# Optimization experiments

Hardware: AMD Instinct MI355X
Metric: run time of the kernel (lower is better)

## Reference

```python
import jax, jax.numpy as jnp
import numpy as np

HEAD_DIM = 128
NUM_BUCKETS = 32
MAX_DISTANCE = 128


def _rel_pos_bucket(seq_len):
    # T5 causal relative-position bucketing (lucidrains flash-pytorch version)
    pos = jnp.arange(seq_len)
    rel = pos[None, :] - pos[:, None]          # k_pos - q_pos
    n = jnp.maximum(-rel, 0)                   # causal: only past distances
    max_exact = NUM_BUCKETS // 2
    is_small = n < max_exact
    n_safe = jnp.maximum(n, 1).astype(jnp.float32)
    val_large = max_exact + (
        jnp.log(n_safe / max_exact) / np.log(MAX_DISTANCE / max_exact)
        * (NUM_BUCKETS - max_exact)
    ).astype(jnp.int32)
    val_large = jnp.minimum(val_large, NUM_BUCKETS - 1)
    return jnp.where(is_small, n, val_large)   # (S, S) int32


def setup_inputs() -> dict:
    key = jax.random.key(0)
    ks = jax.random.split(key, 10)
    B, S, D, I = 4, 2048, 768, 1536
    s = 0.02
    return {
        "x": jax.random.normal(ks[0], (B, S, D), jnp.float32),
        "v_W": jax.random.normal(ks[1], (D, I), jnp.float32) * s,
        "v_b": jnp.zeros((I,), jnp.float32),
        "g_W": jax.random.normal(ks[2], (D, I), jnp.float32) * s,
        "g_b": jnp.zeros((I,), jnp.float32),
        "in_W": jax.random.normal(ks[3], (D, HEAD_DIM), jnp.float32) * s,
        "in_b": jnp.zeros((HEAD_DIM,), jnp.float32),
        "q_gamma": jax.random.normal(ks[4], (HEAD_DIM,), jnp.float32) * s,
        "q_beta": jnp.zeros((HEAD_DIM,), jnp.float32),
        "k_gamma": jax.random.normal(ks[5], (HEAD_DIM,), jnp.float32) * s,
        "k_beta": jnp.zeros((HEAD_DIM,), jnp.float32),
        "out_W": jax.random.normal(ks[6], (I, D), jnp.float32) * s,
        "out_b": jnp.zeros((D,), jnp.float32),
        "rel_emb": jax.random.normal(ks[7], (NUM_BUCKETS, 1), jnp.float32) * s,
    }


def reference(x, v_W, v_b, g_W, g_b, in_W, in_b,
              q_gamma, q_beta, k_gamma, k_beta, out_W, out_b, rel_emb):
    silu = jax.nn.silu
    S = x.shape[1]
    v = silu(x @ v_W + v_b)                    # (B, S, I)
    gate = silu(x @ g_W + g_b)                 # (B, S, I)
    base = silu(x @ in_W + in_b)               # (B, S, 128)
    q = base * q_gamma + q_beta
    k = base * k_gamma + k_beta
    # scores scaled by sqrt(v dim) per torch code (v.size(-1) = inner_dim)
    attn = jnp.einsum('bns,bms->bnm', q, k) / jnp.sqrt(jnp.float32(v.shape[-1]))
    bias = rel_emb[_rel_pos_bucket(S), 0] * np.sqrt(HEAD_DIM)  # (S, S)
    attn = attn + bias
    causal = jnp.triu(jnp.ones((S, S), bool), 1)
    attn = jnp.where(causal, 0.0, attn)        # masked_fill to 0 before relu^2
    attn = jnp.square(jax.nn.relu(attn))       # ReLU^2 attention (no softmax)
    o = jnp.einsum('bnm,bme->bne', attn, v) * gate
    return o @ out_W + out_b                   # (B, S, D)
```

## Files before the change

kernel.cpp:

```cpp
#include <hip/hip_runtime.h>


typedef short short8 __attribute__((ext_vector_type(8)));
typedef float f32x4 __attribute__((ext_vector_type(4)));
typedef unsigned short us4 __attribute__((ext_vector_type(4)));
typedef float fl4 __attribute__((ext_vector_type(4)));

__device__ __forceinline__ unsigned short f2bf(float f) {
  unsigned u = __builtin_bit_cast(unsigned, f);
  u += 0x7FFFu + ((u >> 16) & 1u);
  return (unsigned short)(u >> 16);
}
__device__ __forceinline__ float bf2f(unsigned short b) {
  return __builtin_bit_cast(float, ((unsigned)b) << 16);
}
__device__ __forceinline__ float silu_f(float x) { return x / (1.0f + __expf(-x)); }

__device__ __forceinline__ void gl_lds16(const void* gp, void* lp) {
  __builtin_amdgcn_global_load_lds((const __attribute__((address_space(1))) void*)gp,
                                   (__attribute__((address_space(3))) void*)lp, 16, 0, 0);
}

__device__ __forceinline__ void stage_bf(const unsigned short* __restrict__ g,
                                         int row_stride, int r0, int ko,
                                         unsigned short* lds, int w, int l) {
#pragma unroll
  for (int c = 0; c < 4; ++c) {
    int e = ((w * 4 + c) << 9) + l * 8;
    gl_lds16(g + (size_t)(r0 + (e >> 6)) * row_stride + (ko + (e & 63)), lds + e);
  }
}
__device__ __forceinline__ void stage_bf64(const unsigned short* __restrict__ g,
                                           int row_stride, int r0, int ko,
                                           unsigned short* lds, int w, int l) {
#pragma unroll
  for (int c = 0; c < 2; ++c) {
    int e = ((w * 2 + c) << 9) + l * 8;
    gl_lds16(g + (size_t)(r0 + (e >> 6)) * row_stride + (ko + (e & 63)), lds + e);
  }
}

__device__ __forceinline__ void mfma_bf(const unsigned short* As, const unsigned short* Bs,
                                        f32x4 acc[4][4], int wm, int wn, int quad, int lc) {
#pragma unroll
  for (int kk = 0; kk < 2; ++kk) {
    short8 af[4], bfr[4];
#pragma unroll
    for (int i = 0; i < 4; ++i)
      af[i] = *(const short8*)&As[(wm + i * 16 + lc) * 64 + kk * 32 + quad * 8];
#pragma unroll
    for (int j = 0; j < 4; ++j)
      bfr[j] = *(const short8*)&Bs[(wn + j * 16 + lc) * 64 + kk * 32 + quad * 8];
#pragma unroll
    for (int i = 0; i < 4; ++i)
#pragma unroll
      for (int j = 0; j < 4; ++j)
        acc[i][j] = __builtin_amdgcn_mfma_f32_16x16x32_bf16(af[i], bfr[j], acc[i][j], 0, 0, 0);
  }
}

__global__ __launch_bounds__(256) void g123_k(
    const unsigned short* __restrict__ X,
    const unsigned short* __restrict__ Wst,
    unsigned short* __restrict__ vt,
    unsigned short* __restrict__ gateT,
    unsigned short* __restrict__ wq,
    unsigned short* __restrict__ wk,
    const float* __restrict__ v_b, const float* __restrict__ g_b,
    const float* __restrict__ in_b, const float* __restrict__ q_g,
    const float* __restrict__ q_be, const float* __restrict__ k_g,
    const float* __restrict__ k_be) {
  __shared__ unsigned short As[2][128 * 64];
  __shared__ unsigned short Bs[2][128 * 64];
  const int t = threadIdx.x, l = t & 63, w = t >> 6;
  const int id = blockIdx.x;
  const int xcd = id & 7, rest = id >> 3;
  const int n = rest % 25, m = (rest / 25) * 8 + xcd;
  const int m0 = m * 128, n0 = n * 128;
  const int wm = (w >> 1) * 64, wn = (w & 1) * 64;
  const int quad = l >> 4, lr = quad * 4, lc = l & 15;

  f32x4 acc[4][4] = {};
  stage_bf(X, 768, m0, 0, As[0], w, l);
  stage_bf(Wst, 768, n0, 0, Bs[0], w, l);
  __syncthreads();
  int cur = 0;
  for (int tt = 1; tt < 12; ++tt) {
    stage_bf(X, 768, m0, tt * 64, As[cur ^ 1], w, l);
    stage_bf(Wst, 768, n0, tt * 64, Bs[cur ^ 1], w, l);
    mfma_bf(As[cur], Bs[cur], acc, wm, wn, quad, lc);
    __syncthreads();
    cur ^= 1;
  }
  mfma_bf(As[cur], Bs[cur], acc, wm, wn, quad, lc);

#pragma unroll
  for (int i = 0; i < 4; ++i) {
    const int gm = m0 + wm + i * 16 + lr;
#pragma unroll
    for (int j = 0; j < 4; ++j) {
      const int gn = n0 + wn + j * 16 + lc;
      f32x4 a = acc[i][j];
      if (n0 < 1536) {
        float bv = v_b[gn];
        us4 pk;
#pragma unroll
        for (int r = 0; r < 4; ++r) pk[r] = f2bf(silu_f(a[r] + bv));
        size_t off = (size_t)(gm >> 11) * (1536 * 2048) + (size_t)gn * 2048 + (gm & 2047);
        *(us4*)&vt[off] = pk;
      } else if (n0 < 3072) {
        float bv = g_b[gn - 1536];
        us4 pk;
#pragma unroll
        for (int r = 0; r < 4; ++r) pk[r] = f2bf(silu_f(a[r] + bv));
        *(us4*)&gateT[(size_t)(gn - 1536) * 8192 + gm] = pk;
      } else {
        int h = gn - 3072;
        float bb = in_b[h], qg = q_g[h], qb = q_be[h], kg = k_g[h], kb = k_be[h];
#pragma unroll
        for (int r = 0; r < 4; ++r) {
          float s = silu_f(a[r] + bb);
          wq[(size_t)(gm + r) * 128 + h] = f2bf(s * qg + qb);
          wk[(size_t)(gm + r) * 128 + h] = f2bf(s * kg + kb);
        }
      }
    }
  }
}

__global__ __launch_bounds__(256) void scores_k(
    const unsigned short* __restrict__ wk, const unsigned short* __restrict__ wq,
    unsigned short* __restrict__ P, const float* __restrict__ btab) {
  __shared__ unsigned short As[128 * 128];
  __shared__ unsigned short Bs[128 * 128];
  const int t = threadIdx.x, l = t & 63, w = t >> 6;
  const int z = blockIdx.z;
  int ti = blockIdx.x;
  int r = (int)((sqrtf((float)(8 * ti + 1)) - 1.0f) * 0.5f);
  if ((r + 1) * (r + 2) / 2 <= ti) ++r;
  int c = ti - r * (r + 1) / 2;
  const int m0 = c * 128, n0 = r * 128;
  const unsigned short* A = wk + (size_t)z * 2048 * 128;
  const unsigned short* Bt = wq + (size_t)z * 2048 * 128;
  unsigned short* Pz = P + (size_t)z * 2048 * 2048;
  const int wm = (w >> 1) * 64, wn = (w & 1) * 64;
  const int quad = l >> 4, lr = quad * 4, lc = l & 15;

#pragma unroll
  for (int cc = 0; cc < 8; ++cc) {
    int e = ((w * 8 + cc) << 9) + l * 8;
    gl_lds16(A + (size_t)(m0 + (e >> 7)) * 128 + (e & 127), As + e);
  }
#pragma unroll
  for (int cc = 0; cc < 8; ++cc) {
    int e = ((w * 8 + cc) << 9) + l * 8;
    gl_lds16(Bt + (size_t)(n0 + (e >> 7)) * 128 + (e & 127), Bs + e);
  }
  __syncthreads();

  f32x4 acc[4][4] = {};
#pragma unroll
  for (int kk = 0; kk < 4; ++kk) {
    short8 af[4], bfr[4];
#pragma unroll
    for (int i = 0; i < 4; ++i)
      af[i] = *(const short8*)&As[(wm + i * 16 + lc) * 128 + kk * 32 + quad * 8];
#pragma unroll
    for (int j = 0; j < 4; ++j)
      bfr[j] = *(const short8*)&Bs[(wn + j * 16 + lc) * 128 + kk * 32 + quad * 8];
#pragma unroll
    for (int i = 0; i < 4; ++i)
#pragma unroll
      for (int j = 0; j < 4; ++j)
        acc[i][j] = __builtin_amdgcn_mfma_f32_16x16x32_bf16(af[i], bfr[j], acc[i][j], 0, 0, 0);
  }

  const float SCALE = 0.025515518153991442f;
#pragma unroll
  for (int i = 0; i < 4; ++i) {
    const int gm = m0 + wm + i * 16 + lr;
#pragma unroll
    for (int j = 0; j < 4; ++j) {
      const int gn = n0 + wn + j * 16 + lc;
      us4 pk;
#pragma unroll
      for (int r2 = 0; r2 < 4; ++r2) {
        int mm = gm + r2;
        float v = 0.0f;
        if (mm <= gn) {
          float tt = fmaf(acc[i][j][r2], SCALE, btab[gn - mm]);
          tt = fmaxf(tt, 0.0f);
          v = tt * tt;
        }
        pk[r2] = f2bf(v);
      }
      *(us4*)&Pz[(size_t)gn * 2048 + gm] = pk;
    }
  }
}

__global__ __launch_bounds__(256) void og_k(
    const unsigned short* __restrict__ Vt,
    const unsigned short* __restrict__ P,
    const unsigned short* __restrict__ gateT,
    unsigned short* __restrict__ og) {
  __shared__ unsigned short As[2][128 * 64];
  __shared__ unsigned short Bs[2][128 * 64];
  const int t = threadIdx.x, l = t & 63, w = t >> 6;
  const int id = blockIdx.x;
  const int bblk = id / 96, rr = id % 96;
  const int xcd = rr & 7, mi = rr >> 3;
  const int half = xcd >> 2, z = xcd & 3;
  const int nt = 15 - 2 * bblk - (half ^ (bblk & 1));
  const int m0 = mi * 128;
  const int n0 = nt * 128;
  const int T = (n0 + 128) >> 6;
  const unsigned short* A = Vt + (size_t)z * 1536 * 2048;
  const unsigned short* B = P + (size_t)z * 2048 * 2048;
  const int wm = (w >> 1) * 64, wn = (w & 1) * 64;
  const int quad = l >> 4, lr = quad * 4, lc = l & 15;

  f32x4 acc[4][4] = {};
  stage_bf(A, 2048, m0, 0, As[0], w, l);
  stage_bf(B, 2048, n0, 0, Bs[0], w, l);
  __syncthreads();
  int cur = 0;
  for (int tt = 1; tt < T; ++tt) {
    stage_bf(A, 2048, m0, tt * 64, As[cur ^ 1], w, l);
    stage_bf(B, 2048, n0, tt * 64, Bs[cur ^ 1], w, l);
    mfma_bf(As[cur], Bs[cur], acc, wm, wn, quad, lc);
    __syncthreads();
    cur ^= 1;
  }
  mfma_bf(As[cur], Bs[cur], acc, wm, wn, quad, lc);

#pragma unroll
  for (int i = 0; i < 4; ++i) {
    const int gm = m0 + wm + i * 16 + lr;
#pragma unroll
    for (int j = 0; j < 4; ++j) {
      const int gn = n0 + wn + j * 16 + lc;
      us4 pk;
#pragma unroll
      for (int r2 = 0; r2 < 4; ++r2) {
        float g = bf2f(gateT[(size_t)(gm + r2) * 8192 + z * 2048 + gn]);
        pk[r2] = f2bf(acc[i][j][r2] * g);
      }
      *(us4*)&og[((size_t)z * 2048 + gn) * 1536 + gm] = pk;
    }
  }
}

__global__ __launch_bounds__(256) void gout_k(
    const unsigned short* __restrict__ A,
    const unsigned short* __restrict__ Bt,
    float* __restrict__ out, const float* __restrict__ o_b) {
  __shared__ unsigned short As[2][64 * 64];
  __shared__ unsigned short Bs[2][128 * 64];
  const int t = threadIdx.x, l = t & 63, w = t >> 6;
  const int id = blockIdx.x;
  const int xcd = id & 7, rest = id >> 3;
  const int m = rest % 12, ng = rest / 12;
  const int m0 = m * 64, n0 = (ng * 8 + xcd) * 128;
  const int wm = (w >> 1) * 32, wn = (w & 1) * 64;
  const int quad = l >> 4, lr = quad * 4, lc = l & 15;

  f32x4 acc[2][4] = {};
  stage_bf64(A, 1536, m0, 0, As[0], w, l);
  stage_bf(Bt, 1536, n0, 0, Bs[0], w, l);
  __syncthreads();
  int cur = 0;
  for (int tt = 1; tt < 24; ++tt) {
    stage_bf64(A, 1536, m0, tt * 64, As[cur ^ 1], w, l);
    stage_bf(Bt, 1536, n0, tt * 64, Bs[cur ^ 1], w, l);
#pragma unroll
    for (int kk = 0; kk < 2; ++kk) {
      short8 af[2], bfr[4];
#pragma unroll
      for (int i = 0; i < 2; ++i)
        af[i] = *(const short8*)&As[cur][(wm + i * 16 + lc) * 64 + kk * 32 + quad * 8];
#pragma unroll
      for (int j = 0; j < 4; ++j)
        bfr[j] = *(const short8*)&Bs[cur][(wn + j * 16 + lc) * 64 + kk * 32 + quad * 8];
#pragma unroll
      for (int i = 0; i < 2; ++i)
#pragma unroll
        for (int j = 0; j < 4; ++j)
          acc[i][j] = __builtin_amdgcn_mfma_f32_16x16x32_bf16(af[i], bfr[j], acc[i][j], 0, 0, 0);
    }
    __syncthreads();
    cur ^= 1;
  }
#pragma unroll
  for (int kk = 0; kk < 2; ++kk) {
    short8 af[2], bfr[4];
#pragma unroll
    for (int i = 0; i < 2; ++i)
      af[i] = *(const short8*)&As[cur][(wm + i * 16 + lc) * 64 + kk * 32 + quad * 8];
#pragma unroll
    for (int j = 0; j < 4; ++j)
      bfr[j] = *(const short8*)&Bs[cur][(wn + j * 16 + lc) * 64 + kk * 32 + quad * 8];
#pragma unroll
    for (int i = 0; i < 2; ++i)
#pragma unroll
      for (int j = 0; j < 4; ++j)
        acc[i][j] = __builtin_amdgcn_mfma_f32_16x16x32_bf16(af[i], bfr[j], acc[i][j], 0, 0, 0);
  }

#pragma unroll
  for (int i = 0; i < 2; ++i) {
    const int gm = m0 + wm + i * 16 + lr;
#pragma unroll
    for (int j = 0; j < 4; ++j) {
      const int gn = n0 + wn + j * 16 + lc;
      fl4 ob = *(const fl4*)&o_b[gm];
      fl4 res;
#pragma unroll
      for (int r2 = 0; r2 < 4; ++r2) res[r2] = acc[i][j][r2] + ob[r2];
      *(fl4*)&out[(size_t)gn * 768 + gm] = res;
    }
  }
}

__global__ void cvt_bf16(const float* __restrict__ in, unsigned short* __restrict__ out, int n) {
  int i = (blockIdx.x * blockDim.x + threadIdx.x) * 4;
  if (i < n) {
    fl4 v = *(const fl4*)&in[i];
    us4 o;
#pragma unroll
    for (int r = 0; r < 4; ++r) o[r] = f2bf(v[r]);
    *(us4*)&out[i] = o;
  }
}

__global__ void transpose_cvt4(const float* __restrict__ s0, unsigned short* __restrict__ d0,
                               const float* __restrict__ s1, unsigned short* __restrict__ d1,
                               const float* __restrict__ s2, unsigned short* __restrict__ d2,
                               const float* __restrict__ s3, unsigned short* __restrict__ d3) {
  __shared__ float tile[32][33];
  const float* in;
  unsigned short* out;
  int K_, N_, bxm, bym;
  switch (blockIdx.z) {
    case 0: in = s0; out = d0; K_ = 768; N_ = 1536; bxm = 48; bym = 24; break;
    case 1: in = s1; out = d1; K_ = 768; N_ = 1536; bxm = 48; bym = 24; break;
    case 2: in = s2; out = d2; K_ = 768; N_ = 128;  bxm = 4;  bym = 24; break;
    default: in = s3; out = d3; K_ = 1536; N_ = 768; bxm = 24; bym = 48; break;
  }
  if ((int)blockIdx.x >= bxm || (int)blockIdx.y >= bym) return;
  int bn = blockIdx.x * 32, bk = blockIdx.y * 32;
  int tx = threadIdx.x, ty = threadIdx.y;
#pragma unroll
  for (int i2 = 0; i2 < 32; i2 += 8)
    tile[ty + i2][tx] = in[(size_t)(bk + ty + i2) * N_ + (bn + tx)];
  __syncthreads();
#pragma unroll
  for (int i2 = 0; i2 < 32; i2 += 8)
    out[(size_t)(bn + ty + i2) * K_ + (bk + tx)] = f2bf(tile[tx][ty + i2]);
}

__global__ void build_bias(const float* __restrict__ rel_emb, float* __restrict__ tab) {
  int d = blockIdx.x * blockDim.x + threadIdx.x;
  if (d < 2048) {
    int bucket;
    if (d < 16) {
      bucket = d;
    } else {
      float n = (float)d;
      int vl = 16 + (int)((logf(n * 0.0625f) / logf(8.0f)) * 16.0f);
      bucket = vl < 31 ? vl : 31;
    }
    tab[d] = rel_emb[bucket] * 11.3137085f;
  }
}

extern "C" void kernel_launch(void* const* d_in, const int* in_sizes, int n_in,
                              void* d_out, int out_size, void* d_ws, size_t ws_size,
                              hipStream_t stream) {
  const float* x    = (const float*)d_in[0];
  const float* vW   = (const float*)d_in[1];
  const float* v_b  = (const float*)d_in[2];
  const float* gW   = (const float*)d_in[3];
  const float* g_b  = (const float*)d_in[4];
  const float* inW  = (const float*)d_in[5];
  const float* in_b = (const float*)d_in[6];
  const float* q_g  = (const float*)d_in[7];
  const float* q_be = (const float*)d_in[8];
  const float* k_g  = (const float*)d_in[9];
  const float* k_be = (const float*)d_in[10];
  const float* oW   = (const float*)d_in[11];
  const float* o_b  = (const float*)d_in[12];
  const float* rel  = (const float*)d_in[13];

  char* p = (char*)d_ws;
  auto alloc = [&](size_t bytes) -> char* {
    char* r = p;
    p += (bytes + 255) & ~(size_t)255;
    return r;
  };
  unsigned short* x_bf   = (unsigned short*)alloc(8192ull * 768 * 2);
  unsigned short* wstack = (unsigned short*)alloc(3200ull * 768 * 2);
  unsigned short* vWt  = wstack;
  unsigned short* gWt  = wstack + 1536ull * 768;
  unsigned short* inWt = wstack + 3072ull * 768;
  unsigned short* oWt  = (unsigned short*)alloc(768ull * 1536 * 2);
  unsigned short* wq   = (unsigned short*)alloc(8192ull * 128 * 2);
  unsigned short* wk   = (unsigned short*)alloc(8192ull * 128 * 2);
  unsigned short* vt   = (unsigned short*)alloc(4ull * 1536 * 2048 * 2);
  unsigned short* gateT= (unsigned short*)alloc(1536ull * 8192 * 2);
  unsigned short* P    = (unsigned short*)alloc(4ull * 2048 * 2048 * 2);
  unsigned short* og   = (unsigned short*)alloc(8192ull * 1536 * 2);
  float* btab          = (float*)alloc(2048 * 4);

  cvt_bf16<<<dim3(6144), dim3(256), 0, stream>>>(x, x_bf, 8192 * 768);
  transpose_cvt4<<<dim3(48, 48, 4), dim3(32, 8), 0, stream>>>(vW, vWt, gW, gWt, inW, inWt, oW, oWt);
  build_bias<<<dim3(8), dim3(256), 0, stream>>>(rel, btab);

  g123_k<<<dim3(1600), 256, 0, stream>>>(x_bf, wstack, vt, gateT, wq, wk,
                                         v_b, g_b, in_b, q_g, q_be, k_g, k_be);
  scores_k<<<dim3(136, 1, 4), 256, 0, stream>>>(wk, wq, P, btab);
  og_k<<<dim3(768), 256, 0, stream>>>(vt, P, gateT, og);
  gout_k<<<dim3(768), 256, 0, stream>>>(oWt, og, (float*)d_out, o_b);
}
```

Baseline: 336.8 us.

## Enlarge g123 M-tile, drop LDS double buffering, fuse bias table build

The projection GEMM now computes 256x128 tiles per block with 8x4 accumulators per wave and launches half as many blocks, with a two-blocks-per-CU occupancy hint. The g123, og and gout kernels drop double-buffered LDS staging in favour of a single buffer with load, sync, compute, sync, which halves LDS use so more blocks can be resident. The bias-table kernel is folded into the transpose kernel as an extra z-slice, removing one launch. The cost is that loads no longer overlap MFMA within a block, so latency hiding relies on running more blocks at once. The larger accumulator set also raises register pressure.

```diff
diff --git a/kernel.cpp b/kernel.cpp
--- a/kernel.cpp
+++ b/kernel.cpp
@@ -30,6 +30,15 @@
     gl_lds16(g + (size_t)(r0 + (e >> 6)) * row_stride + (ko + (e & 63)), lds + e);
   }
 }
+__device__ __forceinline__ void stage_bf256(const unsigned short* __restrict__ g,
+                                            int row_stride, int r0, int ko,
+                                            unsigned short* lds, int w, int l) {
+#pragma unroll
+  for (int c = 0; c < 8; ++c) {
+    int e = ((w * 8 + c) << 9) + l * 8;
+    gl_lds16(g + (size_t)(r0 + (e >> 6)) * row_stride + (ko + (e & 63)), lds + e);
+  }
+}
 __device__ __forceinline__ void stage_bf64(const unsigned short* __restrict__ g,
                                            int row_stride, int r0, int ko,
                                            unsigned short* lds, int w, int l) {
@@ -59,7 +68,7 @@
   }
 }
 
-__global__ __launch_bounds__(256) void g123_k(
+__global__ __launch_bounds__(256, 2) void g123_k(
     const unsigned short* __restrict__ X,
     const unsigned short* __restrict__ Wst,
     unsigned short* __restrict__ vt,
@@ -70,32 +79,41 @@
     const float* __restrict__ in_b, const float* __restrict__ q_g,
     const float* __restrict__ q_be, const float* __restrict__ k_g,
     const float* __restrict__ k_be) {
-  __shared__ unsigned short As[2][128 * 64];
-  __shared__ unsigned short Bs[2][128 * 64];
+  __shared__ unsigned short As[256 * 64];
+  __shared__ unsigned short Bs[128 * 64];
   const int t = threadIdx.x, l = t & 63, w = t >> 6;
   const int id = blockIdx.x;
   const int xcd = id & 7, rest = id >> 3;
   const int n = rest % 25, m = (rest / 25) * 8 + xcd;
-  const int m0 = m * 128, n0 = n * 128;
-  const int wm = (w >> 1) * 64, wn = (w & 1) * 64;
+  const int m0 = m * 256, n0 = n * 128;
+  const int wm = (w >> 1) * 128, wn = (w & 1) * 64;
   const int quad = l >> 4, lr = quad * 4, lc = l & 15;
 
-  f32x4 acc[4][4] = {};
-  stage_bf(X, 768, m0, 0, As[0], w, l);
-  stage_bf(Wst, 768, n0, 0, Bs[0], w, l);
-  __syncthreads();
-  int cur = 0;
-  for (int tt = 1; tt < 12; ++tt) {
-    stage_bf(X, 768, m0, tt * 64, As[cur ^ 1], w, l);
-    stage_bf(Wst, 768, n0, tt * 64, Bs[cur ^ 1], w, l);
-    mfma_bf(As[cur], Bs[cur], acc, wm, wn, quad, lc);
-    __syncthreads();
-    cur ^= 1;
-  }
-  mfma_bf(As[cur], Bs[cur], acc, wm, wn, quad, lc);
-
-#pragma unroll
-  for (int i = 0; i < 4; ++i) {
+  f32x4 acc[8][4] = {};
+  for (int ko = 0; ko < 768; ko += 64) {
+    stage_bf256(X, 768, m0, ko, As, w, l);
+    stage_bf(Wst, 768, n0, ko, Bs, w, l);
+    __syncthreads();
+#pragma unroll
+    for (int kk = 0; kk < 2; ++kk) {
+      short8 af[8], bfr[4];
+#pragma unroll
+      for (int i = 0; i < 8; ++i)
+        af[i] = *(const short8*)&As[(wm + i * 16 + lc) * 64 + kk * 32 + quad * 8];
+#pragma unroll
+      for (int j = 0; j < 4; ++j)
+        bfr[j] = *(const short8*)&Bs[(wn + j * 16 + lc) * 64 + kk * 32 + quad * 8];
+#pragma unroll
+      for (int i = 0; i < 8; ++i)
+#pragma unroll
+        for (int j = 0; j < 4; ++j)
+          acc[i][j] = __builtin_amdgcn_mfma_f32_16x16x32_bf16(af[i], bfr[j], acc[i][j], 0, 0, 0);
+    }
+    __syncthreads();
+  }
+
+#pragma unroll
+  for (int i = 0; i < 8; ++i) {
     const int gm = m0 + wm + i * 16 + lr;
 #pragma unroll
     for (int j = 0; j < 4; ++j) {
@@ -204,8 +222,8 @@
     const unsigned short* __restrict__ P,
     const unsigned short* __restrict__ gateT,
     unsigned short* __restrict__ og) {
-  __shared__ unsigned short As[2][128 * 64];
-  __shared__ unsigned short Bs[2][128 * 64];
+  __shared__ unsigned short As[128 * 64];
+  __shared__ unsigned short Bs[128 * 64];
   const int t = threadIdx.x, l = t & 63, w = t >> 6;
   const int id = blockIdx.x;
   const int bblk = id / 96, rr = id % 96;
@@ -214,26 +232,20 @@
   const int nt = 15 - 2 * bblk - (half ^ (bblk & 1));
   const int m0 = mi * 128;
   const int n0 = nt * 128;
-  const int T = (n0 + 128) >> 6;
+  const int kend = n0 + 128;
   const unsigned short* A = Vt + (size_t)z * 1536 * 2048;
   const unsigned short* B = P + (size_t)z * 2048 * 2048;
   const int wm = (w >> 1) * 64, wn = (w & 1) * 64;
   const int quad = l >> 4, lr = quad * 4, lc = l & 15;
 
   f32x4 acc[4][4] = {};
-  stage_bf(A, 2048, m0, 0, As[0], w, l);
-  stage_bf(B, 2048, n0, 0, Bs[0], w, l);
-  __syncthreads();
-  int cur = 0;
-  for (int tt = 1; tt < T; ++tt) {
-    stage_bf(A, 2048, m0, tt * 64, As[cur ^ 1], w, l);
-    stage_bf(B, 2048, n0, tt * 64, Bs[cur ^ 1], w, l);
-    mfma_bf(As[cur], Bs[cur], acc, wm, wn, quad, lc);
-    __syncthreads();
-    cur ^= 1;
-  }
-  mfma_bf(As[cur], Bs[cur], acc, wm, wn, quad, lc);
-
+  for (int ko = 0; ko < kend; ko += 64) {
+    stage_bf(A, 2048, m0, ko, As, w, l);
+    stage_bf(B, 2048, n0, ko, Bs, w, l);
+    __syncthreads();
+    mfma_bf(As, Bs, acc, wm, wn, quad, lc);
+    __syncthreads();
+  }
 #pragma unroll
   for (int i = 0; i < 4; ++i) {
     const int gm = m0 + wm + i * 16 + lr;
@@ -255,8 +267,8 @@
     const unsigned short* __restrict__ A,
     const unsigned short* __restrict__ Bt,
     float* __restrict__ out, const float* __restrict__ o_b) {
-  __shared__ unsigned short As[2][64 * 64];
-  __shared__ unsigned short Bs[2][128 * 64];
+  __shared__ unsigned short As[64 * 64];
+  __shared__ unsigned short Bs[128 * 64];
   const int t = threadIdx.x, l = t & 63, w = t >> 6;
   const int id = blockIdx.x;
   const int xcd = id & 7, rest = id >> 3;
@@ -266,22 +278,19 @@
   const int quad = l >> 4, lr = quad * 4, lc = l & 15;
 
   f32x4 acc[2][4] = {};
-  stage_bf64(A, 1536, m0, 0, As[0], w, l);
-  stage_bf(Bt, 1536, n0, 0, Bs[0], w, l);
-  __syncthreads();
-  int cur = 0;
-  for (int tt = 1; tt < 24; ++tt) {
-    stage_bf64(A, 1536, m0, tt * 64, As[cur ^ 1], w, l);
-    stage_bf(Bt, 1536, n0, tt * 64, Bs[cur ^ 1], w, l);
+  for (int ko = 0; ko < 1536; ko += 64) {
+    stage_bf64(A, 1536, m0, ko, As, w, l);
+    stage_bf(Bt, 1536, n0, ko, Bs, w, l);
+    __syncthreads();
 #pragma unroll
     for (int kk = 0; kk < 2; ++kk) {
       short8 af[2], bfr[4];
 #pragma unroll
       for (int i = 0; i < 2; ++i)
-        af[i] = *(const short8*)&As[cur][(wm + i * 16 + lc) * 64 + kk * 32 + quad * 8];
+        af[i] = *(const short8*)&As[(wm + i * 16 + lc) * 64 + kk * 32 + quad * 8];
 #pragma unroll
       for (int j = 0; j < 4; ++j)
-        bfr[j] = *(const short8*)&Bs[cur][(wn + j * 16 + lc) * 64 + kk * 32 + quad * 8];
+        bfr[j] = *(const short8*)&Bs[(wn + j * 16 + lc) * 64 + kk * 32 + quad * 8];
 #pragma unroll
       for (int i = 0; i < 2; ++i)
 #pragma unroll
@@ -289,24 +298,7 @@
           acc[i][j] = __builtin_amdgcn_mfma_f32_16x16x32_bf16(af[i], bfr[j], acc[i][j], 0, 0, 0);
     }
     __syncthreads();
-    cur ^= 1;
-  }
-#pragma unroll
-  for (int kk = 0; kk < 2; ++kk) {
-    short8 af[2], bfr[4];
-#pragma unroll
-    for (int i = 0; i < 2; ++i)
-      af[i] = *(const short8*)&As[cur][(wm + i * 16 + lc) * 64 + kk * 32 + quad * 8];
-#pragma unroll
-    for (int j = 0; j < 4; ++j)
-      bfr[j] = *(const short8*)&Bs[cur][(wn + j * 16 + lc) * 64 + kk * 32 + quad * 8];
-#pragma unroll
-    for (int i = 0; i < 2; ++i)
-#pragma unroll
-      for (int j = 0; j < 4; ++j)
-        acc[i][j] = __builtin_amdgcn_mfma_f32_16x16x32_bf16(af[i], bfr[j], acc[i][j], 0, 0, 0);
-  }
-
+  }
 #pragma unroll
   for (int i = 0; i < 2; ++i) {
     const int gm = m0 + wm + i * 16 + lr;
@@ -336,7 +328,26 @@
 __global__ void transpose_cvt4(const float* __restrict__ s0, unsigned short* __restrict__ d0,
                                const float* __restrict__ s1, unsigned short* __restrict__ d1,
                                const float* __restrict__ s2, unsigned short* __restrict__ d2,
-                               const float* __restrict__ s3, unsigned short* __restrict__ d3) {
+                               const float* __restrict__ s3, unsigned short* __restrict__ d3,
+                               const float* __restrict__ rel_emb, float* __restrict__ tab) {
+  if (blockIdx.z == 4) {
+    if (blockIdx.x == 0 && blockIdx.y == 0) {
+      int d = threadIdx.y * 32 + threadIdx.x;
+#pragma unroll
+      for (int rep = 0; rep < 8; ++rep, d += 256) {
+        int bucket;
+        if (d < 16) {
+          bucket = d;
+        } else {
+          float n = (float)d;
+          int vl = 16 + (int)((logf(n * 0.0625f) / logf(8.0f)) * 16.0f);
+          bucket = vl < 31 ? vl : 31;
+        }
+        tab[d] = rel_emb[bucket] * 11.3137085f;
+      }
+    }
+    return;
+  }
   __shared__ float tile[32][33];
   const float* in;
   unsigned short* out;
@@ -357,21 +368,6 @@
 #pragma unroll
   for (int i2 = 0; i2 < 32; i2 += 8)
     out[(size_t)(bn + ty + i2) * K_ + (bk + tx)] = f2bf(tile[tx][ty + i2]);
-}
-
-__global__ void build_bias(const float* __restrict__ rel_emb, float* __restrict__ tab) {
-  int d = blockIdx.x * blockDim.x + threadIdx.x;
-  if (d < 2048) {
-    int bucket;
-    if (d < 16) {
-      bucket = d;
-    } else {
-      float n = (float)d;
-      int vl = 16 + (int)((logf(n * 0.0625f) / logf(8.0f)) * 16.0f);
-      bucket = vl < 31 ? vl : 31;
-    }
-    tab[d] = rel_emb[bucket] * 11.3137085f;
-  }
 }
 
 extern "C" void kernel_launch(void* const* d_in, const int* in_sizes, int n_in,
@@ -413,11 +409,11 @@
   float* btab          = (float*)alloc(2048 * 4);
 
   cvt_bf16<<<dim3(6144), dim3(256), 0, stream>>>(x, x_bf, 8192 * 768);
-  transpose_cvt4<<<dim3(48, 48, 4), dim3(32, 8), 0, stream>>>(vW, vWt, gW, gWt, inW, inWt, oW, oWt);
-  build_bias<<<dim3(8), dim3(256), 0, stream>>>(rel, btab);
-
-  g123_k<<<dim3(1600), 256, 0, stream>>>(x_bf, wstack, vt, gateT, wq, wk,
-                                         v_b, g_b, in_b, q_g, q_be, k_g, k_be);
+  transpose_cvt4<<<dim3(48, 48, 5), dim3(32, 8), 0, stream>>>(vW, vWt, gW, gWt, inW, inWt,
+                                                              oW, oWt, rel, btab);
+
+  g123_k<<<dim3(800), 256, 0, stream>>>(x_bf, wstack, vt, gateT, wq, wk,
+                                        v_b, g_b, in_b, q_g, q_be, k_g, k_be);
   scores_k<<<dim3(136, 1, 4), 256, 0, stream>>>(wk, wq, P, btab);
   og_k<<<dim3(768), 256, 0, stream>>>(vt, P, gateT, og);
   gout_k<<<dim3(768), 256, 0, stream>>>(oWt, og, (float*)d_out, o_b);
```

Result: faster. 320.3 us (-4.9%).
